# Performance work log

Measured on AMD Instinct MI355X. Metric: run time of the kernel, lower is better.

## Reference

```python
import jax, jax.numpy as jnp
import numpy as np

B, T, H, W, C = 2, 8, 20, 36, 512
NH = 4
HD = C // NH
WS = (5, 9)
EXP = (2, 4)              # window_size // 2
KP = (5, 9)               # focal unfold kernel for level k=0
PADP = (2, 4)
T2T_K, T2T_S, T2T_P = (7, 7), (3, 3), (3, 3)
FFN_HD = 1960
NWH, NWW = H // WS[0], W // WS[1]   # 4, 4
WAREA = WS[0] * WS[1]               # 45


def _valid_ind_rolled():
    wh, ww = WS
    eh, ew = EXP
    m = np.ones((4, wh, ww), np.float32)
    m[0, :wh - eh, :ww - ew] = 0   # tl
    m[1, :wh - eh, ew:] = 0        # tr
    m[2, eh:, :ww - ew] = 0        # bl
    m[3, eh:, ew:] = 0             # br
    return jnp.asarray(np.nonzero(m.reshape(-1))[0])

VALID_ROLLED = _valid_ind_rolled()  # (120,)


def unfold(x, k, s, p):
    # x: (N, Cc, Hh, Ww) -> (N, Cc*kh*kw, L); matches torch.nn.Unfold layout (c slowest).
    N, Cc, Hh, Ww = x.shape
    kh, kw = k; sh, sw = s; ph, pw = p
    xp = jnp.pad(x, ((0, 0), (0, 0), (ph, ph), (pw, pw)))
    oh = (Hh + 2 * ph - kh) // sh + 1
    ow = (Ww + 2 * pw - kw) // sw + 1
    cols = [xp[:, :, i:i + oh * sh:sh, j:j + ow * sw:sw]
            for i in range(kh) for j in range(kw)]
    patches = jnp.stack(cols, axis=2)            # (N, Cc, kh*kw, oh, ow)
    return patches.reshape(N, Cc * kh * kw, oh * ow)


def fold(patches, out_hw, k, s, p):
    # inverse of unfold (overlap-add), matches torch F.fold.
    N = patches.shape[0]
    kh, kw = k; sh, sw = s; ph, pw = p
    Hh, Ww = out_hw
    oh = (Hh + 2 * ph - kh) // sh + 1
    ow = (Ww + 2 * pw - kw) // sw + 1
    Cc = patches.shape[1] // (kh * kw)
    pr = patches.reshape(N, Cc, kh, kw, oh, ow)
    out = jnp.zeros((N, Cc, Hh + 2 * ph, Ww + 2 * pw), patches.dtype)
    for i in range(kh):
        for j in range(kw):
            out = out.at[:, :, i:i + oh * sh:sh, j:j + ow * sw:sw].add(pr[:, :, i, j])
    return out[:, :, ph:ph + Hh, pw:pw + Ww]


def layer_norm(x, g, b):
    mu = jnp.mean(x, -1, keepdims=True)
    var = jnp.var(x, -1, keepdims=True)
    return (x - mu) * jax.lax.rsqrt(var + 1e-5) * g + b


def win_part(x):
    # (B,T,H,W,C) -> (B*nW, T*wh*ww, C)
    b = x.shape[0]
    x = x.reshape(b, T, NWH, WS[0], NWW, WS[1], C)
    return x.transpose(0, 2, 4, 1, 3, 5, 6).reshape(-1, T * WAREA, C)


def to_heads(w):
    return w.reshape(-1, T, WAREA, NH, HD).transpose(0, 3, 1, 2, 4).reshape(-1, NH, T * WAREA, HD)


def block_forward(x, g1, be1, wqkv, bqkv, wproj, bproj, wpool, bpool, g2, be2, w1, bf1, w2, bf2, out_h, out_w):
    shortcut = x
    xn = layer_norm(x, g1, be1)

    # ---- coarser (pooled) focal level, k=0 (focal_level=2) ----
    wnr = xn.reshape(B, T, NWH, WS[0], NWW, WS[1], C).transpose(0, 2, 4, 1, 3, 5, 6)
    wnr = wnr.reshape(B, NWH, NWW, T, WAREA, C)
    pooled = jnp.einsum('bhwtnc,n->bhwtc', wnr, wpool) + bpool   # (B,NWH,NWW,T,C)

    # ---- window attention ----
    qkv = xn @ wqkv + bqkv                                       # (B,T,H,W,3C)
    q, k, v = jnp.split(qkv, 3, axis=-1)
    qw = to_heads(win_part(q)) * (HD ** -0.5)
    kw_, vw = to_heads(win_part(k)), to_heads(win_part(v))

    def rolled(t):
        parts = []
        for sh, sw in ((-EXP[0], -EXP[1]), (-EXP[0], EXP[1]), (EXP[0], -EXP[1]), (EXP[0], EXP[1])):
            r = jnp.roll(t, (sh, sw), axis=(2, 3))
            parts.append(win_part(r).reshape(-1, T, WAREA, NH, HD))
        cat = jnp.concatenate(parts, axis=2)                     # (B*nW, T, 4*warea, NH, HD)
        cat = jnp.take(cat.transpose(0, 3, 1, 2, 4), VALID_ROLLED, axis=3)
        return cat.reshape(-1, NH, T * VALID_ROLLED.shape[0], HD)

    k_rolled = jnp.concatenate([kw_, rolled(k)], axis=2)         # (B*nW, NH, T*165, HD)
    v_rolled = jnp.concatenate([vw, rolled(v)], axis=2)

    # pooled keys/values via focal unfold
    xp = pooled.transpose(0, 3, 1, 2, 4)                          # (B,T,NWH,NWW,C)
    qkv_p = xp @ wqkv + bqkv
    kp, vp = qkv_p[..., C:2 * C], qkv_p[..., 2 * C:]

    def unfold_kv(t):
        t = t.transpose(0, 1, 4, 2, 3).reshape(B * T, C, NWH, NWW)
        u = unfold(t, KP, (1, 1), PADP)                           # (B*T, C*45, L)
        L = u.shape[-1]
        u = u.reshape(B, T, C, KP[0], KP[1], L).transpose(0, 5, 1, 3, 4, 2)
        u = u.reshape(B * L, T, KP[0] * KP[1], NH, HD).transpose(0, 3, 1, 2, 4)
        return u.reshape(B * L, NH, T * KP[0] * KP[1], HD)

    k_all = jnp.concatenate([k_rolled, unfold_kv(kp)], axis=2)
    v_all = jnp.concatenate([v_rolled, unfold_kv(vp)], axis=2)

    attn = jnp.einsum('wnqd,wnkd->wnqk', qw, k_all)               # (B*nW, NH, T*45, N)

    # validity mask for pooled context (zero-padded unfold positions -> -100)
    ones = jnp.ones((T, 1, NWH, NWW), x.dtype)
    um = unfold(ones, KP, (1, 1), PADP)                           # (T, 45, L)
    L = um.shape[-1]
    mvals = jnp.where(um.reshape(T, KP[0] * KP[1], L).transpose(2, 0, 1).reshape(L, -1) == 0,
                      jnp.asarray(-100.0, x.dtype), jnp.asarray(0.0, x.dtype))
    n_rolled = k_rolled.shape[2]
    mask_cols = jnp.concatenate([jnp.zeros((L, n_rolled), x.dtype), mvals], axis=1)
    attn = attn + jnp.tile(mask_cols, (B, 1))[:, None, None, :]

    attn = jax.nn.softmax(attn, axis=-1)
    out = jnp.einsum('wnqk,wnkd->wnqd', attn, v_all)
    out = out.transpose(0, 2, 1, 3).reshape(-1, T * WAREA, C) @ wproj + bproj

    # window reverse + residual
    out = out.reshape(B, NWH, NWW, T, WS[0], WS[1], C)
    out = out.transpose(0, 3, 1, 4, 2, 5, 6).reshape(B, T, H, W, C)
    x = shortcut + out

    # ---- FusionFeedForward (fold/unfold re-normalized MLP) ----
    y = layer_norm(x, g2, be2).reshape(B, T * H * W, C)
    h = y @ w1 + bf1                                              # (B, n, 1960)
    nvec = ((out_h + 2 * T2T_P[0] - T2T_K[0]) // T2T_S[0] + 1) * \
           ((out_w + 2 * T2T_P[1] - T2T_K[1]) // T2T_S[1] + 1)
    bt = (B * T * H * W) // nvec
    norm_p = jnp.ones((bt, T2T_K[0] * T2T_K[1], nvec), x.dtype)
    norm_f = fold(norm_p, (out_h, out_w), T2T_K, T2T_S, T2T_P)    # (bt,1,out_h,out_w)
    h_f = fold(h.reshape(bt, nvec, FFN_HD).transpose(0, 2, 1), (out_h, out_w), T2T_K, T2T_S, T2T_P)
    h = unfold(h_f / norm_f, T2T_K, T2T_S, T2T_P).transpose(0, 2, 1).reshape(B, T * H * W, FFN_HD)
    h = jax.nn.gelu(h, approximate=False) @ w2 + bf2
    return x + h.reshape(B, T, H, W, C)


def setup_inputs() -> dict:
    key = jax.random.key(0)
    ks = jax.random.split(key, 8)
    s = 0.02
    return dict(
        x=jax.random.normal(ks[0], (B, T, H, W, C), jnp.float32),
        g1=jnp.ones((C,), jnp.float32),
        be1=jnp.zeros((C,), jnp.float32),
        wqkv=jax.random.normal(ks[1], (C, 3 * C), jnp.float32) * s,
        bqkv=jnp.zeros((3 * C,), jnp.float32),
        wproj=jax.random.normal(ks[2], (C, C), jnp.float32) * s,
        bproj=jnp.zeros((C,), jnp.float32),
        wpool=jnp.full((WAREA,), 1.0 / WAREA, jnp.float32),
        bpool=jnp.zeros((1,), jnp.float32),
        g2=jnp.ones((C,), jnp.float32),
        be2=jnp.zeros((C,), jnp.float32),
        w1=jax.random.normal(ks[3], (C, FFN_HD), jnp.float32) * s,
        bf1=jnp.zeros((FFN_HD,), jnp.float32),
        w2=jax.random.normal(ks[4], (FFN_HD, C), jnp.float32) * s,
        bf2=jnp.zeros((C,), jnp.float32),
        out_h=60,
        out_w=108,
    )


def reference(x, g1, be1, wqkv, bqkv, wproj, bproj, wpool, bpool, g2, be2, w1, bf1, w2, bf2, out_h, out_w):
    return block_forward(x, g1, be1, wqkv, bqkv, wproj, bproj, wpool, bpool,
                         g2, be2, w1, bf1, w2, bf2, out_h, out_w)
```

## Files before the change

kernel.cpp:

```cpp
#include <hip/hip_runtime.h>
#include <hip/hip_bf16.h>
#include <math.h>

typedef __hip_bfloat16 bf16;
typedef __attribute__((ext_vector_type(8))) short bf16x8;
typedef __attribute__((ext_vector_type(4))) float f32x4;

#define DEVI __device__ __forceinline__

#define C_ 512
#define NH_ 4
#define NTOK 11520
#define NKEY 1680
#define NRK 120
#define FFN_ 1960
#define POOLED_FLAG 0x40000000

DEVI float bfu(unsigned u) { return __uint_as_float(u << 16); }
DEVI float ldf(const bf16* p) { return __bfloat162float(*p); }
DEVI float ldf(const float* p) { return *p; }
DEVI void stw(bf16* p, float v) { *p = __float2bfloat16(v); }
DEVI void stw(float* p, float v) { *p = v; }
DEVI unsigned short f2bs(float f) { bf16 h = __float2bfloat16(f); return *(unsigned short*)&h; }
DEVI unsigned pk2(float a, float b) {
  return (unsigned)f2bs(a) | ((unsigned)f2bs(b) << 16);
}

template <int DT> DEVI float ldw(const void* p, size_t i) {
  if (DT == 0) return __bfloat162float(((const bf16*)p)[i]);
  else         return ((const float*)p)[i];
}

DEVI void gload_lds16(const void* g, void* l) {
  __builtin_amdgcn_global_load_lds(
      (const __attribute__((address_space(1))) void*)g,
      (__attribute__((address_space(3))) void*)l, 16, 0, 0);
}

__global__ void k_detect(const void* __restrict__ g1, int* __restrict__ flag) {
  if (threadIdx.x == 0) {
    const unsigned short* p = (const unsigned short*)g1;
    *flag = (p[0] == 0x3F80u) ? 0 : 1;
  }
}

__global__ void k_prep(int* __restrict__ table) {
  if (threadIdx.x == 0) {
    int cnt = 0;
    for (int p = 0; p < 4; p++)
      for (int wi = 0; wi < 5; wi++)
        for (int wj = 0; wj < 9; wj++) {
          bool invalid;
          if (p == 0)      invalid = (wi < 3) && (wj < 5);
          else if (p == 1) invalid = (wi < 3) && (wj >= 4);
          else if (p == 2) invalid = (wi >= 2) && (wj < 5);
          else             invalid = (wi >= 2) && (wj >= 4);
          if (!invalid) table[cnt++] = p * 45 + wi * 9 + wj;
        }
  }
}

__global__ void k_ksrc(const int* __restrict__ vtab, int* __restrict__ ksrc) {
  int idx = blockIdx.x * 256 + threadIdx.x;
  if (idx >= 32 * NKEY) return;
  int w = idx / NKEY, j = idx % NKEY;
  int b = w >> 4, nh = (w >> 2) & 3, nw = w & 3;
  int val;
  if (j < 360) {
    int t = j / 45, pos = j % 45, wi = pos / 9, wj2 = pos % 9;
    val = ((b * 8 + t) * 20 + nh * 5 + wi) * 36 + nw * 9 + wj2;
  } else if (j < 1320) {
    int jj = j - 360;
    int t = jj / 120, r = jj % 120;
    int id = vtab[r];
    int p = id / 45, pos = id % 45, wi = pos / 9, wj2 = pos % 9;
    int sh = (p < 2) ? -2 : 2;
    int sw = (p & 1) ? 4 : -4;
    int hh = nh * 5 + wi - sh;
    if (hh < 0) hh += 20; else if (hh >= 20) hh -= 20;
    int ww2 = nw * 9 + wj2 - sw;
    if (ww2 < 0) ww2 += 36; else if (ww2 >= 36) ww2 -= 36;
    val = ((b * 8 + t) * 20 + hh) * 36 + ww2;
  } else {
    int jj = j - 1320;
    int t = jj / 45, kidx = jj % 45, ki = kidx / 9, kj = kidx % 9;
    int snh = nh + ki - 2, snw = nw + kj - 4;
    if (snh < 0 || snh >= 4 || snw < 0 || snw >= 4) val = -1;
    else val = POOLED_FLAG | ((b * 8 + t) * 16 + snh * 4 + snw);
  }
  ksrc[idx] = val;
}

template <int DT>
__global__ void k_wcvt(const int* __restrict__ dflag, const void* __restrict__ in,
                       bf16* __restrict__ out, int K, int N, int Npad) {
  if (*dflag != DT) return;
  int idx = blockIdx.x * 256 + threadIdx.x;
  if (idx >= Npad * K) return;
  int n = idx / K, k = idx % K;
  float v = (n < N) ? ldw<DT>(in, (size_t)k * N + n) : 0.f;
  out[idx] = __float2bfloat16(v);
}

template <int DT>
__global__ void k_bcvt(const int* __restrict__ dflag, const void* __restrict__ in,
                       float* __restrict__ out, int n) {
  if (*dflag != DT) return;
  int i = blockIdx.x * 256 + threadIdx.x;
  if (i < n) out[i] = ldw<DT>(in, i);
}

template <int DT, typename InT>
__global__ void k_ln(const int* __restrict__ dflag, const InT* __restrict__ xin,
                     const void* __restrict__ g, const void* __restrict__ be,
                     bf16* __restrict__ out) {
  if (*dflag != DT) return;
  const int tok = blockIdx.x;
  const int tid = threadIdx.x;
  const size_t base = (size_t)tok * C_;
  float v0 = ldf(xin + base + tid);
  float v1 = ldf(xin + base + tid + 256);
  float s = v0 + v1, ss = v0 * v0 + v1 * v1;
#pragma unroll
  for (int o = 32; o; o >>= 1) { s += __shfl_xor(s, o); ss += __shfl_xor(ss, o); }
  __shared__ float sh[10];
  const int lane = tid & 63, wv = tid >> 6;
  if (lane == 0) { sh[wv] = s; sh[4 + wv] = ss; }
  __syncthreads();
  if (tid == 0) {
    float a = sh[0] + sh[1] + sh[2] + sh[3];
    float q = sh[4] + sh[5] + sh[6] + sh[7];
    float mu = a * (1.0f / C_);
    float var = q * (1.0f / C_) - mu * mu;
    sh[8] = mu; sh[9] = rsqrtf(fmaxf(var, 0.f) + 1e-5f);
  }
  __syncthreads();
  float mu = sh[8], inv = sh[9];
  stw(out + base + tid,
      (v0 - mu) * inv * ldw<DT>(g, tid) + ldw<DT>(be, tid));
  stw(out + base + tid + 256,
      (v1 - mu) * inv * ldw<DT>(g, tid + 256) + ldw<DT>(be, tid + 256));
}

template <int DT>
__global__ void k_pool(const int* __restrict__ dflag, const bf16* __restrict__ xn,
                       const void* __restrict__ wpool, const void* __restrict__ bpool,
                       float* __restrict__ pooled) {
  if (*dflag != DT) return;
  int idx = blockIdx.x * blockDim.x + threadIdx.x;
  if (idx >= 256 * C_) return;
  int c = idx & (C_ - 1);
  int fw = idx >> 9;
  int nw = fw & 3, nh = (fw >> 2) & 3;
  int bt = fw >> 4;
  float acc = ldw<DT>(bpool, 0);
  for (int wi = 0; wi < 5; wi++) {
    int hh = nh * 5 + wi;
    const bf16* base = xn + (((size_t)(bt * 20 + hh)) * 36 + nw * 9) * C_ + c;
    for (int wj = 0; wj < 9; wj++)
      acc += __bfloat162float(base[(size_t)wj * C_]) * ldw<DT>(wpool, wi * 9 + wj);
  }
  pooled[idx] = acc;
}

template <int DT>
__global__ void k_gemm_small(const int* __restrict__ dflag, const float* __restrict__ A,
                             const void* __restrict__ Bw, const void* __restrict__ bias,
                             float* __restrict__ Cc) {
  if (*dflag != DT) return;
  int n = blockIdx.x * blockDim.x + threadIdx.x;
  int m = blockIdx.y;
  if (n >= 1536) return;
  float acc = ldw<DT>(bias, n);
  const float* a = A + (size_t)m * C_;
  for (int k = 0; k < C_; k++)
    acc += a[k] * ldw<DT>(Bw, (size_t)k * 1536 + n);
  Cc[(size_t)m * 1536 + n] = acc;
}

template <int DT, int RES, typename OutT>
__global__ __launch_bounds__(256) void k_gemm_m(const int* __restrict__ dflag,
                                                const bf16* __restrict__ A,
                                                const bf16* __restrict__ Bt,
                                                const float* __restrict__ bias,
                                                const void* __restrict__ resid,
                                                OutT* __restrict__ out,
                                                int M, int N, int K) {
  if (dflag && *dflag != DT) return;
  __shared__ __align__(16) unsigned short As[128 * 32];
  __shared__ __align__(16) unsigned short Bs[128 * 32];
  const int tid = threadIdx.x;
  const int lane = tid & 63, wid = tid >> 6;
  const int r15 = lane & 15, quad = lane >> 4;
  const int wm = wid >> 1, wn = wid & 1;
  const int m0 = blockIdx.y * 128, n0 = blockIdx.x * 128;

  f32x4 acc[4][4];
#pragma unroll
  for (int i = 0; i < 4; i++)
#pragma unroll
    for (int j = 0; j < 4; j++)
#pragma unroll
      for (int e = 0; e < 4; e++) acc[i][j][e] = 0.f;

  const int lrow = lane >> 2, lcol = (lane & 3) * 8;

  for (int k0 = 0; k0 < K; k0 += 32) {
    int rem = K - k0;
    if (rem >= 32) {
      const bf16* ga = A + (size_t)(m0 + wid * 32 + lrow) * K + k0 + lcol;
      gload_lds16(ga, &As[wid * 1024]);
      gload_lds16(ga + (size_t)16 * K, &As[wid * 1024 + 512]);
      const bf16* gb = Bt + (size_t)(n0 + wid * 32 + lrow) * K + k0 + lcol;
      gload_lds16(gb, &Bs[wid * 1024]);
      gload_lds16(gb + (size_t)16 * K, &Bs[wid * 1024 + 512]);
    } else {
      int r = tid >> 2, c = (tid & 3) * 8;
      uint4 z = make_uint4(0, 0, 0, 0);
      uint4 a0 = z, a1 = z, b0 = z, b1 = z;
      if (c < rem) {
        a0 = *(const uint4*)(A + (size_t)(m0 + r) * K + k0 + c);
        a1 = *(const uint4*)(A + (size_t)(m0 + r + 64) * K + k0 + c);
        b0 = *(const uint4*)(Bt + (size_t)(n0 + r) * K + k0 + c);
        b1 = *(const uint4*)(Bt + (size_t)(n0 + r + 64) * K + k0 + c);
      }
      *(uint4*)&As[r * 32 + c] = a0;
      *(uint4*)&As[(r + 64) * 32 + c] = a1;
      *(uint4*)&Bs[r * 32 + c] = b0;
      *(uint4*)&Bs[(r + 64) * 32 + c] = b1;
    }
    __syncthreads();

    bf16x8 af[4], bfr[4];
#pragma unroll
    for (int mf = 0; mf < 4; mf++)
      af[mf] = *(const bf16x8*)&As[(wm * 64 + mf * 16 + r15) * 32 + quad * 8];
#pragma unroll
    for (int nf = 0; nf < 4; nf++)
      bfr[nf] = *(const bf16x8*)&Bs[(wn * 64 + nf * 16 + r15) * 32 + quad * 8];
#pragma unroll
    for (int mf = 0; mf < 4; mf++)
#pragma unroll
      for (int nf = 0; nf < 4; nf++)
        acc[mf][nf] = __builtin_amdgcn_mfma_f32_16x16x32_bf16(af[mf], bfr[nf],
                                                              acc[mf][nf], 0, 0, 0);
    __syncthreads();
  }

#pragma unroll
  for (int nf = 0; nf < 4; nf++) {
    int n = n0 + wn * 64 + nf * 16 + r15;
    if (n >= N) continue;
    float bv = bias[n];
#pragma unroll
    for (int mf = 0; mf < 4; mf++) {
      int mb = m0 + wm * 64 + mf * 16 + quad * 4;
#pragma unroll
      for (int e = 0; e < 4; e++) {
        size_t off = (size_t)(mb + e) * N + n;
        float v = acc[mf][nf][e] + bv;
        if (RES == 1) v += ldw<DT>(resid, off);
        else if (RES == 2) v += ((const float*)resid)[off];
        stw(out + off, v);
      }
    }
  }
}

#define KT 64
#define KPAD 136
#define VPAD 72
__global__ __launch_bounds__(768) void k_attn_m(const bf16* __restrict__ qkv,
                                                const float* __restrict__ qkvp,
                                                const int* __restrict__ ksrc,
                                                bf16* __restrict__ ao) {
  __shared__ int ks_l[NKEY];
  __shared__ __align__(16) unsigned short ktl[2][KT * KPAD];
  __shared__ __align__(16) unsigned short vtl[2][128 * VPAD];
  __shared__ __align__(16) unsigned short ptl[12 * 16 * VPAD];
  __shared__ float maskv[2][KT];

  const int tid = threadIdx.x;
  const int lane = tid & 63, wid = tid >> 6;
  const int r15 = lane & 15, quad = lane >> 4;
  const int w = blockIdx.x, qt = blockIdx.y, n = blockIdx.z;
  const int b = w >> 4, nh = (w >> 2) & 3, nw = w & 3;
  const unsigned short* qkvs = (const unsigned short*)qkv;

  for (int j = tid; j < NKEY; j += 768) ks_l[j] = ksrc[w * NKEY + j];

  bf16x8 qf[4];
  {
    int qw = qt * 192 + wid * 16 + r15;
    int qc2 = qw < 360 ? qw : 359;
    int t = qc2 / 45, pos = qc2 % 45, wi = pos / 9, wj = pos % 9;
    int tok = ((b * 8 + t) * 20 + nh * 5 + wi) * 36 + nw * 9 + wj;
    const unsigned short* qp = qkvs + (size_t)tok * 1536 + n * 128 + quad * 8;
#pragma unroll
    for (int c = 0; c < 4; c++)
      qf[c] = *(const bf16x8*)(qp + c * 32);
  }

  f32x4 of[8];
#pragma unroll
  for (int nt = 0; nt < 8; nt++)
#pragma unroll
    for (int e = 0; e < 4; e++) of[nt][e] = 0.f;
  float m_[4], l_[4];
#pragma unroll
  for (int e = 0; e < 4; e++) { m_[e] = -1e30f; l_[e] = 0.f; }

  unsigned short* ptw = &ptl[wid * 16 * VPAD];

  const bool isK = (wid < 4);
  const int kr = tid >> 2, kp = tid & 3;
  const int vr = lane, vp8 = wid - 4;
  uint4 kreg[4], vreg[2];
  float mreg = -30000.f;

  auto load_tile = [&](int j0) {
    int cnt = NKEY - j0; if (cnt > KT) cnt = KT;
    if (isK) {
      int s0 = (kr < cnt) ? ks_l[j0 + kr] : -1;
      mreg = (s0 < 0) ? -30000.f : 0.f;
      if (s0 < 0) {
        kreg[0] = kreg[1] = kreg[2] = kreg[3] = make_uint4(0, 0, 0, 0);
      } else if (s0 & POOLED_FLAG) {
        const float* kf = qkvp + (size_t)(s0 & 0x3FFFFFFF) * 1536 + 512 + n * 128 + kp * 32;
#pragma unroll
        for (int i = 0; i < 4; i++) {
          float4 f0 = ((const float4*)kf)[2 * i], f1 = ((const float4*)kf)[2 * i + 1];
          kreg[i] = make_uint4(pk2(f0.x, f0.y), pk2(f0.z, f0.w),
                               pk2(f1.x, f1.y), pk2(f1.z, f1.w));
        }
      } else {
        const uint4* kq = (const uint4*)(qkvs + (size_t)s0 * 1536 + 512 + n * 128 + kp * 32);
#pragma unroll
        for (int i = 0; i < 4; i++) kreg[i] = kq[i];
      }
    } else {
      int s1 = (vr < cnt) ? ks_l[j0 + vr] : -1;
      if (s1 < 0) {
        vreg[0] = vreg[1] = make_uint4(0, 0, 0, 0);
      } else if (s1 & POOLED_FLAG) {
        const float* vf = qkvp + (size_t)(s1 & 0x3FFFFFFF) * 1536 + 1024 + n * 128 + vp8 * 16;
#pragma unroll
        for (int i = 0; i < 2; i++) {
          float4 f0 = ((const float4*)vf)[2 * i], f1 = ((const float4*)vf)[2 * i + 1];
          vreg[i] = make_uint4(pk2(f0.x, f0.y), pk2(f0.z, f0.w),
                               pk2(f1.x, f1.y), pk2(f1.z, f1.w));
        }
      } else {
        const uint4* vq = (const uint4*)(qkvs + (size_t)s1 * 1536 + 1024 + n * 128 + vp8 * 16);
        vreg[0] = vq[0];
        vreg[1] = vq[1];
      }
    }
  };

  auto store_tile = [&](int buf) {
    if (isK) {
      if (kp == 0) maskv[buf][kr] = mreg;
      unsigned short* kb = &ktl[buf][0];
#pragma unroll
      for (int i = 0; i < 4; i++)
        *(uint4*)&kb[kr * KPAD + kp * 32 + i * 8] = kreg[i];
    } else {
      unsigned short* vb = &vtl[buf][0];
#pragma unroll
      for (int i = 0; i < 2; i++) {
        uint4 u = vreg[i];
        int d0 = vp8 * 16 + i * 8;
        vb[(d0 + 0) * VPAD + vr] = (unsigned short)(u.x & 0xFFFFu);
        vb[(d0 + 1) * VPAD + vr] = (unsigned short)(u.x >> 16);
        vb[(d0 + 2) * VPAD + vr] = (unsigned short)(u.y & 0xFFFFu);
        vb[(d0 + 3) * VPAD + vr] = (unsigned short)(u.y >> 16);
        vb[(d0 + 4) * VPAD + vr] = (unsigned short)(u.z & 0xFFFFu);
        vb[(d0 + 5) * VPAD + vr] = (unsigned short)(u.z >> 16);
        vb[(d0 + 6) * VPAD + vr] = (unsigned short)(u.w & 0xFFFFu);
        vb[(d0 + 7) * VPAD + vr] = (unsigned short)(u.w >> 16);
      }
    }
  };

  __syncthreads();
  load_tile(0);
  store_tile(0);
  load_tile(KT);
  __syncthreads();

  int cur = 0, j0 = 0;
  while (true) {
    int nxt = j0 + KT;
    if (nxt < NKEY) {
      store_tile(cur ^ 1);
      if (nxt + KT < NKEY) load_tile(nxt + KT);
    }

    const unsigned short* ktc = &ktl[cur][0];
    const unsigned short* vtc = &vtl[cur][0];
    const float* mkc = maskv[cur];

    f32x4 sf[4];
#pragma unroll
    for (int ft = 0; ft < 4; ft++)
#pragma unroll
      for (int e = 0; e < 4; e++) sf[ft][e] = 0.f;
#pragma unroll
    for (int kc = 0; kc < 4; kc++) {
      bf16x8 a = qf[kc];
#pragma unroll
      for (int ft = 0; ft < 4; ft++) {
        bf16x8 bb = *(const bf16x8*)&ktc[(ft * 16 + r15) * KPAD + kc * 32 + quad * 8];
        sf[ft] = __builtin_amdgcn_mfma_f32_16x16x32_bf16(a, bb, sf[ft], 0, 0, 0);
      }
    }
    const float scl = 0.088388347648318447f;
#pragma unroll
    for (int ft = 0; ft < 4; ft++) {
      float mk = mkc[ft * 16 + r15];
#pragma unroll
      for (int e = 0; e < 4; e++) sf[ft][e] = sf[ft][e] * scl + mk;
    }
    float tm[4], rs[4];
#pragma unroll
    for (int e = 0; e < 4; e++) {
      float v = fmaxf(fmaxf(sf[0][e], sf[1][e]), fmaxf(sf[2][e], sf[3][e]));
#pragma unroll
      for (int o = 1; o < 16; o <<= 1) v = fmaxf(v, __shfl_xor(v, o));
      tm[e] = v;
    }
#pragma unroll
    for (int e = 0; e < 4; e++) {
      float mn = fmaxf(m_[e], tm[e]);
      float alpha = __expf(m_[e] - mn);
      m_[e] = mn;
      rs[e] = 0.f;
#pragma unroll
      for (int ft = 0; ft < 4; ft++) {
        float pv = __expf(sf[ft][e] - mn);
        rs[e] += pv;
        ptw[(quad * 4 + e) * VPAD + ft * 16 + r15] = f2bs(pv);
      }
#pragma unroll
      for (int o = 1; o < 16; o <<= 1) rs[e] += __shfl_xor(rs[e], o);
      l_[e] = l_[e] * alpha + rs[e];
#pragma unroll
      for (int nt = 0; nt < 8; nt++) of[nt][e] *= alpha;
    }
#pragma unroll
    for (int kc = 0; kc < 2; kc++) {
      bf16x8 pa = *(const bf16x8*)&ptw[r15 * VPAD + kc * 32 + quad * 8];
#pragma unroll
      for (int nt = 0; nt < 8; nt++) {
        bf16x8 vb = *(const bf16x8*)&vtc[(nt * 16 + r15) * VPAD + kc * 32 + quad * 8];
        of[nt] = __builtin_amdgcn_mfma_f32_16x16x32_bf16(pa, vb, of[nt], 0, 0, 0);
      }
    }

    if (nxt >= NKEY) break;
    __syncthreads();
    cur ^= 1; j0 = nxt;
  }

#pragma unroll
  for (int e = 0; e < 4; e++) {
    int qw = qt * 192 + wid * 16 + quad * 4 + e;
    if (qw >= 360) continue;
    float inv = 1.0f / l_[e];
    int t = qw / 45, pos = qw % 45, wi = pos / 9, wj = pos % 9;
    int tok = ((b * 8 + t) * 20 + nh * 5 + wi) * 36 + nw * 9 + wj;
    bf16* op = ao + (size_t)tok * 512 + n * 128 + r15;
#pragma unroll
    for (int nt = 0; nt < 8; nt++)
      stw(op + nt * 16, of[nt][e] * inv);
  }
}

__global__ void k_fold(const bf16* __restrict__ h1, float* __restrict__ hf) {
  int idx = blockIdx.x * 256 + threadIdx.x;
  if (idx >= 16 * 40 * 60 * 108) return;
  int x = idx % 108;
  int tmp = idx / 108;
  int y = tmp % 60; tmp /= 60;
  int c = tmp % 40;
  int bt = tmp / 40;
  float sum = 0.f;
  int cnt = 0;
  for (int ki = y % 3; ki < 7; ki += 3) {
    int num = y + 3 - ki;
    if (num < 0) continue;
    int oh = num / 3;
    if (oh >= 20) continue;
    for (int kj = x % 3; kj < 7; kj += 3) {
      int num2 = x + 3 - kj;
      if (num2 < 0) continue;
      int ow = num2 / 3;
      if (ow >= 36) continue;
      sum += __bfloat162float(
          h1[(size_t)(bt * 720 + oh * 36 + ow) * FFN_ + c * 49 + ki * 7 + kj]);
      cnt++;
    }
  }
  hf[idx] = sum / (float)cnt;
}

__global__ void k_unfold_gelu(const float* __restrict__ hf, bf16* __restrict__ h2) {
  int idx = blockIdx.x * 256 + threadIdx.x;
  if (idx >= NTOK * FFN_) return;
  int f = idx % FFN_;
  int token = idx / FFN_;
  int c = f / 49, k = f % 49, ki = k / 7, kj = k % 7;
  int bt = token / 720, vec = token % 720;
  int oh = vec / 36, ow = vec % 36;
  int y = oh * 3 + ki - 3, x = ow * 3 + kj - 3;
  float v = 0.f;
  if (y >= 0 && y < 60 && x >= 0 && x < 108)
    v = hf[((size_t)(bt * 40 + c) * 60 + y) * 108 + x];
  float g = 0.5f * v * (1.0f + erff(v * 0.70710678118654752f));
  stw(h2 + idx, g);
}

extern "C" void kernel_launch(void* const* d_in, const int* in_sizes, int n_in,
                              void* d_out, int out_size, void* d_ws, size_t ws_size,
                              hipStream_t stream) {
  (void)in_sizes; (void)n_in; (void)out_size; (void)ws_size;
  const void* x     = d_in[0];
  const void* g1    = d_in[1];
  const void* be1   = d_in[2];
  const void* wqkv  = d_in[3];
  const void* bqkv  = d_in[4];
  const void* wproj = d_in[5];
  const void* bproj = d_in[6];
  const void* wpool = d_in[7];
  const void* bpool = d_in[8];
  const void* g2    = d_in[9];
  const void* be2   = d_in[10];
  const void* w1    = d_in[11];
  const void* bf1   = d_in[12];
  const void* w2    = d_in[13];
  const void* bf2   = d_in[14];

  char* ws = (char*)d_ws;
  size_t off = 0;
  auto alloc = [&](size_t bytes) -> void* {
    void* p = ws + off;
    off += (bytes + 255) & ~(size_t)255;
    return p;
  };

  int*   dflag  = (int*)  alloc(256);
  int*   vtab   = (int*)  alloc(NRK * sizeof(int));
  int*   ksrc   = (int*)  alloc((size_t)32 * NKEY * sizeof(int));
  bf16*  buf2   = (bf16*) alloc((size_t)NTOK * FFN_ * 2);
  float* pooled = (float*)alloc((size_t)256 * C_ * 4);
  float* qkvp   = (float*)alloc((size_t)256 * 1536 * 4);
  float* x2     = (float*)alloc((size_t)NTOK * C_ * 4);
  float* hf     = (float*)alloc((size_t)16 * 40 * 60 * 108 * 4);
  bf16*  wqkv_t = (bf16*) alloc((size_t)1536 * 512 * 2);
  bf16*  wproj_t= (bf16*) alloc((size_t)512 * 512 * 2);
  bf16*  w1_t   = (bf16*) alloc((size_t)2048 * 512 * 2);
  bf16*  w2_t   = (bf16*) alloc((size_t)512 * FFN_ * 2);
  float* bqkv_f = (float*)alloc(1536 * 4);
  float* bproj_f= (float*)alloc(512 * 4);
  float* bf1_f  = (float*)alloc(FFN_ * 4);
  float* bf2_f  = (float*)alloc(512 * 4);

  bf16* buf1 = (bf16*)d_out;
  bf16* xn = buf1;
  bf16* ao = buf1;
  bf16* y  = buf1;
  bf16* qkv = buf2;
  bf16* h1  = buf2;

  k_detect<<<1, 64, 0, stream>>>(g1, dflag);
  k_prep<<<1, 64, 0, stream>>>(vtab);
  k_ksrc<<<(32 * NKEY) / 256, 256, 0, stream>>>(vtab, ksrc);

  k_wcvt<0><<<(1536 * 512) / 256, 256, 0, stream>>>(dflag, wqkv, wqkv_t, 512, 1536, 1536);
  k_wcvt<1><<<(1536 * 512) / 256, 256, 0, stream>>>(dflag, wqkv, wqkv_t, 512, 1536, 1536);
  k_wcvt<0><<<(512 * 512) / 256, 256, 0, stream>>>(dflag, wproj, wproj_t, 512, 512, 512);
  k_wcvt<1><<<(512 * 512) / 256, 256, 0, stream>>>(dflag, wproj, wproj_t, 512, 512, 512);
  k_wcvt<0><<<(2048 * 512) / 256, 256, 0, stream>>>(dflag, w1, w1_t, 512, FFN_, 2048);
  k_wcvt<1><<<(2048 * 512) / 256, 256, 0, stream>>>(dflag, w1, w1_t, 512, FFN_, 2048);
  k_wcvt<0><<<(512 * FFN_ + 255) / 256, 256, 0, stream>>>(dflag, w2, w2_t, FFN_, 512, 512);
  k_wcvt<1><<<(512 * FFN_ + 255) / 256, 256, 0, stream>>>(dflag, w2, w2_t, FFN_, 512, 512);
  k_bcvt<0><<<6, 256, 0, stream>>>(dflag, bqkv, bqkv_f, 1536);
  k_bcvt<1><<<6, 256, 0, stream>>>(dflag, bqkv, bqkv_f, 1536);
  k_bcvt<0><<<2, 256, 0, stream>>>(dflag, bproj, bproj_f, 512);
  k_bcvt<1><<<2, 256, 0, stream>>>(dflag, bproj, bproj_f, 512);
  k_bcvt<0><<<8, 256, 0, stream>>>(dflag, bf1, bf1_f, FFN_);
  k_bcvt<1><<<8, 256, 0, stream>>>(dflag, bf1, bf1_f, FFN_);
  k_bcvt<0><<<2, 256, 0, stream>>>(dflag, bf2, bf2_f, 512);
  k_bcvt<1><<<2, 256, 0, stream>>>(dflag, bf2, bf2_f, 512);

  k_ln<0, bf16><<<NTOK, 256, 0, stream>>>(dflag, (const bf16*)x, g1, be1, xn);
  k_ln<1, float><<<NTOK, 256, 0, stream>>>(dflag, (const float*)x, g1, be1, xn);

  k_pool<0><<<512, 256, 0, stream>>>(dflag, xn, wpool, bpool, pooled);
  k_pool<1><<<512, 256, 0, stream>>>(dflag, xn, wpool, bpool, pooled);

  k_gemm_m<0, 0, bf16><<<dim3(12, 90), 256, 0, stream>>>(
      nullptr, xn, wqkv_t, bqkv_f, nullptr, qkv, NTOK, 1536, 512);

  k_gemm_small<0><<<dim3(6, 256), 256, 0, stream>>>(dflag, pooled, wqkv, bqkv, qkvp);
  k_gemm_small<1><<<dim3(6, 256), 256, 0, stream>>>(dflag, pooled, wqkv, bqkv, qkvp);

  k_attn_m<<<dim3(32, 2, NH_), 768, 0, stream>>>(qkv, qkvp, ksrc, ao);

  k_gemm_m<0, 1, float><<<dim3(4, 90), 256, 0, stream>>>(
      dflag, ao, wproj_t, bproj_f, x, x2, NTOK, 512, 512);
  k_gemm_m<1, 1, float><<<dim3(4, 90), 256, 0, stream>>>(
      dflag, ao, wproj_t, bproj_f, x, x2, NTOK, 512, 512);

  k_ln<0, float><<<NTOK, 256, 0, stream>>>(dflag, x2, g2, be2, y);
  k_ln<1, float><<<NTOK, 256, 0, stream>>>(dflag, x2, g2, be2, y);

  k_gemm_m<0, 0, bf16><<<dim3(16, 90), 256, 0, stream>>>(
      nullptr, y, w1_t, bf1_f, nullptr, h1, NTOK, FFN_, 512);

  k_fold<<<(16 * 40 * 60 * 108) / 256, 256, 0, stream>>>(h1, hf);

  k_unfold_gelu<<<(NTOK * FFN_) / 256, 256, 0, stream>>>(hf, h1);

  k_gemm_m<0, 2, bf16><<<dim3(4, 90), 256, 0, stream>>>(
      dflag, h1, w2_t, bf2_f, x2, (bf16*)d_out, NTOK, 512, FFN_);
  k_gemm_m<1, 2, float><<<dim3(4, 90), 256, 0, stream>>>(
      dflag, h1, w2_t, bf2_f, x2, (float*)d_out, NTOK, 512, FFN_);
}
```

Before: 584.7 us.

## Unify pooled keys into bf16 qkv buffer, tile weight transpose, lazy softmax rescale

The pooled-token projection now writes bf16 rows directly after the main qkv rows, with an extra zero row, so the attention kernel loads every key and value row the same way without branches or float-to-bf16 packing. The weight conversion kernels become LDS-tiled transposes so both reads and writes are coalesced. The small pooled GEMM reuses each weight load across 8 rows held in shared memory. The attention softmax skips the rescale when the running max grows by less than a threshold, moves the row-sum reduction out of the loop, and raises wave priority around the MFMA blocks. The lazy rescale relies on bounded exponent growth and could change numerics slightly, and pooled K/V are now stored in bf16 instead of fp32.

```diff
diff --git a/kernel.cpp b/kernel.cpp
--- a/kernel.cpp
+++ b/kernel.cpp
@@ -14,17 +14,13 @@
 #define NKEY 1680
 #define NRK 120
 #define FFN_ 1960
-#define POOLED_FLAG 0x40000000
-
-DEVI float bfu(unsigned u) { return __uint_as_float(u << 16); }
+#define ZROW (NTOK + 256)
+
 DEVI float ldf(const bf16* p) { return __bfloat162float(*p); }
 DEVI float ldf(const float* p) { return *p; }
 DEVI void stw(bf16* p, float v) { *p = __float2bfloat16(v); }
 DEVI void stw(float* p, float v) { *p = v; }
 DEVI unsigned short f2bs(float f) { bf16 h = __float2bfloat16(f); return *(unsigned short*)&h; }
-DEVI unsigned pk2(float a, float b) {
-  return (unsigned)f2bs(a) | ((unsigned)f2bs(b) << 16);
-}
 
 template <int DT> DEVI float ldw(const void* p, size_t i) {
   if (DT == 0) return __bfloat162float(((const bf16*)p)[i]);
@@ -86,7 +82,7 @@
     int t = jj / 45, kidx = jj % 45, ki = kidx / 9, kj = kidx % 9;
     int snh = nh + ki - 2, snw = nw + kj - 4;
     if (snh < 0 || snh >= 4 || snw < 0 || snw >= 4) val = -1;
-    else val = POOLED_FLAG | ((b * 8 + t) * 16 + snh * 4 + snw);
+    else val = NTOK + (b * 8 + t) * 16 + snh * 4 + snw;
   }
   ksrc[idx] = val;
 }
@@ -95,11 +91,25 @@
 __global__ void k_wcvt(const int* __restrict__ dflag, const void* __restrict__ in,
                        bf16* __restrict__ out, int K, int N, int Npad) {
   if (*dflag != DT) return;
-  int idx = blockIdx.x * 256 + threadIdx.x;
-  if (idx >= Npad * K) return;
-  int n = idx / K, k = idx % K;
-  float v = (n < N) ? ldw<DT>(in, (size_t)k * N + n) : 0.f;
-  out[idx] = __float2bfloat16(v);
+  __shared__ float t[64][65];
+  const int n0 = blockIdx.x * 64;
+  const int k0 = blockIdx.y * 64;
+  const int tx = threadIdx.x & 63, tg = threadIdx.x >> 6;
+#pragma unroll
+  for (int r = 0; r < 16; r++) {
+    int k = k0 + r * 4 + tg;
+    int nn = n0 + tx;
+    float v = (k < K && nn < N) ? ldw<DT>(in, (size_t)k * N + nn) : 0.f;
+    t[r * 4 + tg][tx] = v;
+  }
+  __syncthreads();
+#pragma unroll
+  for (int r = 0; r < 16; r++) {
+    int nn = n0 + r * 4 + tg;
+    int k = k0 + tx;
+    if (nn < Npad && k < K)
+      out[(size_t)nn * K + k] = __float2bfloat16(t[tx][r * 4 + tg]);
+  }
 }
 
 template <int DT>
@@ -108,6 +118,10 @@
   if (*dflag != DT) return;
   int i = blockIdx.x * 256 + threadIdx.x;
   if (i < n) out[i] = ldw<DT>(in, i);
+}
+
+__global__ void k_zrow(bf16* __restrict__ p) {
+  p[blockIdx.x * 256 + threadIdx.x] = __float2bfloat16(0.f);
 }
 
 template <int DT, typename InT>
@@ -166,16 +180,26 @@
 template <int DT>
 __global__ void k_gemm_small(const int* __restrict__ dflag, const float* __restrict__ A,
                              const void* __restrict__ Bw, const void* __restrict__ bias,
-                             float* __restrict__ Cc) {
+                             bf16* __restrict__ Cc) {
   if (*dflag != DT) return;
-  int n = blockIdx.x * blockDim.x + threadIdx.x;
-  int m = blockIdx.y;
-  if (n >= 1536) return;
-  float acc = ldw<DT>(bias, n);
-  const float* a = A + (size_t)m * C_;
-  for (int k = 0; k < C_; k++)
-    acc += a[k] * ldw<DT>(Bw, (size_t)k * 1536 + n);
-  Cc[(size_t)m * 1536 + n] = acc;
+  __shared__ float As[8][512];
+  const int n = blockIdx.x * 256 + threadIdx.x;
+  const int m0 = blockIdx.y * 8;
+  for (int i = threadIdx.x; i < 8 * 512; i += 256)
+    As[i >> 9][i & 511] = A[(size_t)(m0 + (i >> 9)) * 512 + (i & 511)];
+  __syncthreads();
+  float acc[8];
+  float bv = ldw<DT>(bias, n);
+#pragma unroll
+  for (int mm = 0; mm < 8; mm++) acc[mm] = bv;
+  for (int k = 0; k < 512; k++) {
+    float b = ldw<DT>(Bw, (size_t)k * 1536 + n);
+#pragma unroll
+    for (int mm = 0; mm < 8; mm++) acc[mm] += As[mm][k] * b;
+  }
+#pragma unroll
+  for (int mm = 0; mm < 8; mm++)
+    Cc[(size_t)(m0 + mm) * 1536 + n] = __float2bfloat16(acc[mm]);
 }
 
 template <int DT, int RES, typename OutT>
@@ -271,7 +295,6 @@
 #define KPAD 136
 #define VPAD 72
 __global__ __launch_bounds__(768) void k_attn_m(const bf16* __restrict__ qkv,
-                                                const float* __restrict__ qkvp,
                                                 const int* __restrict__ ksrc,
                                                 bf16* __restrict__ ao) {
   __shared__ int ks_l[NKEY];
@@ -323,38 +346,16 @@
     if (isK) {
       int s0 = (kr < cnt) ? ks_l[j0 + kr] : -1;
       mreg = (s0 < 0) ? -30000.f : 0.f;
-      if (s0 < 0) {
-        kreg[0] = kreg[1] = kreg[2] = kreg[3] = make_uint4(0, 0, 0, 0);
-      } else if (s0 & POOLED_FLAG) {
-        const float* kf = qkvp + (size_t)(s0 & 0x3FFFFFFF) * 1536 + 512 + n * 128 + kp * 32;
-#pragma unroll
-        for (int i = 0; i < 4; i++) {
-          float4 f0 = ((const float4*)kf)[2 * i], f1 = ((const float4*)kf)[2 * i + 1];
-          kreg[i] = make_uint4(pk2(f0.x, f0.y), pk2(f0.z, f0.w),
-                               pk2(f1.x, f1.y), pk2(f1.z, f1.w));
-        }
-      } else {
-        const uint4* kq = (const uint4*)(qkvs + (size_t)s0 * 1536 + 512 + n * 128 + kp * 32);
-#pragma unroll
-        for (int i = 0; i < 4; i++) kreg[i] = kq[i];
-      }
+      int row = (s0 < 0) ? ZROW : s0;
+      const uint4* kq = (const uint4*)(qkvs + (size_t)row * 1536 + 512 + n * 128 + kp * 32);
+#pragma unroll
+      for (int i = 0; i < 4; i++) kreg[i] = kq[i];
     } else {
       int s1 = (vr < cnt) ? ks_l[j0 + vr] : -1;
-      if (s1 < 0) {
-        vreg[0] = vreg[1] = make_uint4(0, 0, 0, 0);
-      } else if (s1 & POOLED_FLAG) {
-        const float* vf = qkvp + (size_t)(s1 & 0x3FFFFFFF) * 1536 + 1024 + n * 128 + vp8 * 16;
-#pragma unroll
-        for (int i = 0; i < 2; i++) {
-          float4 f0 = ((const float4*)vf)[2 * i], f1 = ((const float4*)vf)[2 * i + 1];
-          vreg[i] = make_uint4(pk2(f0.x, f0.y), pk2(f0.z, f0.w),
-                               pk2(f1.x, f1.y), pk2(f1.z, f1.w));
-        }
-      } else {
-        const uint4* vq = (const uint4*)(qkvs + (size_t)s1 * 1536 + 1024 + n * 128 + vp8 * 16);
-        vreg[0] = vq[0];
-        vreg[1] = vq[1];
-      }
+      int row = (s1 < 0) ? ZROW : s1;
+      const uint4* vq = (const uint4*)(qkvs + (size_t)row * 1536 + 1024 + n * 128 + vp8 * 16);
+      vreg[0] = vq[0];
+      vreg[1] = vq[1];
     }
   };
 
@@ -406,6 +407,7 @@
     for (int ft = 0; ft < 4; ft++)
 #pragma unroll
       for (int e = 0; e < 4; e++) sf[ft][e] = 0.f;
+    __builtin_amdgcn_s_setprio(1);
 #pragma unroll
     for (int kc = 0; kc < 4; kc++) {
       bf16x8 a = qf[kc];
@@ -415,6 +417,7 @@
         sf[ft] = __builtin_amdgcn_mfma_f32_16x16x32_bf16(a, bb, sf[ft], 0, 0, 0);
       }
     }
+    __builtin_amdgcn_s_setprio(0);
     const float scl = 0.088388347648318447f;
 #pragma unroll
     for (int ft = 0; ft < 4; ft++) {
@@ -422,32 +425,47 @@
 #pragma unroll
       for (int e = 0; e < 4; e++) sf[ft][e] = sf[ft][e] * scl + mk;
     }
-    float tm[4], rs[4];
+    float tm[4];
+    bool grow = false;
 #pragma unroll
     for (int e = 0; e < 4; e++) {
       float v = fmaxf(fmaxf(sf[0][e], sf[1][e]), fmaxf(sf[2][e], sf[3][e]));
 #pragma unroll
       for (int o = 1; o < 16; o <<= 1) v = fmaxf(v, __shfl_xor(v, o));
       tm[e] = v;
-    }
-#pragma unroll
-    for (int e = 0; e < 4; e++) {
-      float mn = fmaxf(m_[e], tm[e]);
-      float alpha = __expf(m_[e] - mn);
-      m_[e] = mn;
-      rs[e] = 0.f;
-#pragma unroll
-      for (int ft = 0; ft < 4; ft++) {
-        float pv = __expf(sf[ft][e] - mn);
-        rs[e] += pv;
-        ptw[(quad * 4 + e) * VPAD + ft * 16 + r15] = f2bs(pv);
+      grow = grow || (v > m_[e] + 8.f);
+    }
+    if (__any(grow)) {
+#pragma unroll
+      for (int e = 0; e < 4; e++) {
+        float mn = fmaxf(m_[e], tm[e]);
+        float alpha = __expf(m_[e] - mn);
+        m_[e] = mn;
+        float rs = 0.f;
+#pragma unroll
+        for (int ft = 0; ft < 4; ft++) {
+          float pv = __expf(sf[ft][e] - mn);
+          rs += pv;
+          ptw[(quad * 4 + e) * VPAD + ft * 16 + r15] = f2bs(pv);
+        }
+        l_[e] = l_[e] * alpha + rs;
+#pragma unroll
+        for (int nt = 0; nt < 8; nt++) of[nt][e] *= alpha;
       }
-#pragma unroll
-      for (int o = 1; o < 16; o <<= 1) rs[e] += __shfl_xor(rs[e], o);
-      l_[e] = l_[e] * alpha + rs[e];
-#pragma unroll
-      for (int nt = 0; nt < 8; nt++) of[nt][e] *= alpha;
-    }
+    } else {
+#pragma unroll
+      for (int e = 0; e < 4; e++) {
+        float rs = 0.f;
+#pragma unroll
+        for (int ft = 0; ft < 4; ft++) {
+          float pv = __expf(sf[ft][e] - m_[e]);
+          rs += pv;
+          ptw[(quad * 4 + e) * VPAD + ft * 16 + r15] = f2bs(pv);
+        }
+        l_[e] += rs;
+      }
+    }
+    __builtin_amdgcn_s_setprio(1);
 #pragma unroll
     for (int kc = 0; kc < 2; kc++) {
       bf16x8 pa = *(const bf16x8*)&ptw[r15 * VPAD + kc * 32 + quad * 8];
@@ -457,12 +475,18 @@
         of[nt] = __builtin_amdgcn_mfma_f32_16x16x32_bf16(pa, vb, of[nt], 0, 0, 0);
       }
     }
+    __builtin_amdgcn_s_setprio(0);
 
     if (nxt >= NKEY) break;
     __syncthreads();
     cur ^= 1; j0 = nxt;
   }
 
+#pragma unroll
+  for (int e = 0; e < 4; e++) {
+#pragma unroll
+    for (int o = 1; o < 16; o <<= 1) l_[e] += __shfl_xor(l_[e], o);
+  }
 #pragma unroll
   for (int e = 0; e < 4; e++) {
     int qw = qt * 192 + wid * 16 + quad * 4 + e;
@@ -554,7 +578,6 @@
   int*   ksrc   = (int*)  alloc((size_t)32 * NKEY * sizeof(int));
   bf16*  buf2   = (bf16*) alloc((size_t)NTOK * FFN_ * 2);
   float* pooled = (float*)alloc((size_t)256 * C_ * 4);
-  float* qkvp   = (float*)alloc((size_t)256 * 1536 * 4);
   float* x2     = (float*)alloc((size_t)NTOK * C_ * 4);
   float* hf     = (float*)alloc((size_t)16 * 40 * 60 * 108 * 4);
   bf16*  wqkv_t = (bf16*) alloc((size_t)1536 * 512 * 2);
@@ -572,19 +595,21 @@
   bf16* y  = buf1;
   bf16* qkv = buf2;
   bf16* h1  = buf2;
+  bf16* qkvpb = buf2 + (size_t)NTOK * 1536;
 
   k_detect<<<1, 64, 0, stream>>>(g1, dflag);
   k_prep<<<1, 64, 0, stream>>>(vtab);
   k_ksrc<<<(32 * NKEY) / 256, 256, 0, stream>>>(vtab, ksrc);
-
-  k_wcvt<0><<<(1536 * 512) / 256, 256, 0, stream>>>(dflag, wqkv, wqkv_t, 512, 1536, 1536);
-  k_wcvt<1><<<(1536 * 512) / 256, 256, 0, stream>>>(dflag, wqkv, wqkv_t, 512, 1536, 1536);
-  k_wcvt<0><<<(512 * 512) / 256, 256, 0, stream>>>(dflag, wproj, wproj_t, 512, 512, 512);
-  k_wcvt<1><<<(512 * 512) / 256, 256, 0, stream>>>(dflag, wproj, wproj_t, 512, 512, 512);
-  k_wcvt<0><<<(2048 * 512) / 256, 256, 0, stream>>>(dflag, w1, w1_t, 512, FFN_, 2048);
-  k_wcvt<1><<<(2048 * 512) / 256, 256, 0, stream>>>(dflag, w1, w1_t, 512, FFN_, 2048);
-  k_wcvt<0><<<(512 * FFN_ + 255) / 256, 256, 0, stream>>>(dflag, w2, w2_t, FFN_, 512, 512);
-  k_wcvt<1><<<(512 * FFN_ + 255) / 256, 256, 0, stream>>>(dflag, w2, w2_t, FFN_, 512, 512);
+  k_zrow<<<6, 256, 0, stream>>>(qkvpb + (size_t)256 * 1536);
+
+  k_wcvt<0><<<dim3(24, 8), 256, 0, stream>>>(dflag, wqkv, wqkv_t, 512, 1536, 1536);
+  k_wcvt<1><<<dim3(24, 8), 256, 0, stream>>>(dflag, wqkv, wqkv_t, 512, 1536, 1536);
+  k_wcvt<0><<<dim3(8, 8), 256, 0, stream>>>(dflag, wproj, wproj_t, 512, 512, 512);
+  k_wcvt<1><<<dim3(8, 8), 256, 0, stream>>>(dflag, wproj, wproj_t, 512, 512, 512);
+  k_wcvt<0><<<dim3(32, 8), 256, 0, stream>>>(dflag, w1, w1_t, 512, FFN_, 2048);
+  k_wcvt<1><<<dim3(32, 8), 256, 0, stream>>>(dflag, w1, w1_t, 512, FFN_, 2048);
+  k_wcvt<0><<<dim3(8, 31), 256, 0, stream>>>(dflag, w2, w2_t, FFN_, 512, 512);
+  k_wcvt<1><<<dim3(8, 31), 256, 0, stream>>>(dflag, w2, w2_t, FFN_, 512, 512);
   k_bcvt<0><<<6, 256, 0, stream>>>(dflag, bqkv, bqkv_f, 1536);
   k_bcvt<1><<<6, 256, 0, stream>>>(dflag, bqkv, bqkv_f, 1536);
   k_bcvt<0><<<2, 256, 0, stream>>>(dflag, bproj, bproj_f, 512);
@@ -603,10 +628,10 @@
   k_gemm_m<0, 0, bf16><<<dim3(12, 90), 256, 0, stream>>>(
       nullptr, xn, wqkv_t, bqkv_f, nullptr, qkv, NTOK, 1536, 512);
 
-  k_gemm_small<0><<<dim3(6, 256), 256, 0, stream>>>(dflag, pooled, wqkv, bqkv, qkvp);
-  k_gemm_small<1><<<dim3(6, 256), 256, 0, stream>>>(dflag, pooled, wqkv, bqkv, qkvp);
-
-  k_attn_m<<<dim3(32, 2, NH_), 768, 0, stream>>>(qkv, qkvp, ksrc, ao);
+  k_gemm_small<0><<<dim3(6, 32), 256, 0, stream>>>(dflag, pooled, wqkv, bqkv, qkvpb);
+  k_gemm_small<1><<<dim3(6, 32), 256, 0, stream>>>(dflag, pooled, wqkv, bqkv, qkvpb);
+
+  k_attn_m<<<dim3(32, 2, NH_), 768, 0, stream>>>(qkv, ksrc, ao);
 
   k_gemm_m<0, 1, float><<<dim3(4, 90), 256, 0, stream>>>(
       dflag, ao, wproj_t, bproj_f, x, x2, NTOK, 512, 512);
```

Result: slower. 601.7 us (+2.9%).
